# Performance work log

Hardware: AMD Instinct MI355X
Metric: run time of the kernel (lower is better)

## Reference

```python
import jax, jax.numpy as jnp
import numpy as np

B, C_IN, H, W = 4, 1536, 64, 64   # SGI input: cat of three 512-ch encoder maps at 64x64
HID, OUT = 1536, 512
N = H * W


def _grid_edge_index(h, w):
    # 4-connected bidirectional grid, matching SGI.grid_edge_index
    idx = np.arange(h * w).reshape(h, w)
    right = np.stack([idx[:, :-1].ravel(), idx[:, 1:].ravel()])
    down = np.stack([idx[:-1, :].ravel(), idx[1:, :].ravel()])
    ei = np.concatenate([right, down, right[::-1], down[::-1]], axis=1)
    return ei.astype(np.int32)


def setup_inputs() -> dict:
    key = jax.random.key(0)
    ks = jax.random.split(key, 7)
    ei = _grid_edge_index(H, W)
    s = 0.02
    return {
        "x":  jax.random.normal(ks[0], (B, C_IN, H, W), jnp.float32),
        "W1": jax.random.normal(ks[1], (C_IN, HID), jnp.float32) * s,
        "b1": jnp.zeros((HID,), jnp.float32),
        "W2": jax.random.normal(ks[2], (HID, OUT), jnp.float32) * s,
        "b2": jnp.zeros((OUT,), jnp.float32),
        "Wl": jax.random.normal(ks[3], (C_IN, OUT), jnp.float32) * s,
        "bl": jnp.zeros((OUT,), jnp.float32),
        "src": jnp.asarray(ei[0]),
        "dst": jnp.asarray(ei[1]),
    }


def _gcn(h_in, Wt, b, src, dst, inv_sqrt_deg, inv_deg):
    # PyG GCNConv: lin -> symmetric-normalized aggregation (with self loops) -> +bias
    h = h_in @ Wt                                   # [B, N, F]
    norm = inv_sqrt_deg[src] * inv_sqrt_deg[dst]    # [E]
    msgs = h[:, src, :] * norm[None, :, None]       # [B, E, F]
    # self-loop contribution has norm 1/deg_i
    agg = (h * inv_deg[None, :, None]).at[:, dst, :].add(msgs)
    return agg + b


def reference(x, W1, b1, W2, b2, Wl, bl, src, dst):
    Bb, C, Hh, Ww = x.shape
    n = Hh * Ww
    # degree including self loop (graph is symmetric)
    deg = jnp.zeros((n,), x.dtype).at[dst].add(1.0) + 1.0
    inv_sqrt_deg = jax.lax.rsqrt(deg)
    inv_deg = 1.0 / deg

    xt = x.reshape(Bb, C, n).transpose(0, 2, 1)     # [B, N, C]
    identity = xt
    origin = xt @ Wl + bl                           # [B, N, OUT]
    h = jax.nn.relu(_gcn(xt, W1, b1, src, dst, inv_sqrt_deg, inv_deg))
    h = _gcn(h + identity, W2, b2, src, dst, inv_sqrt_deg, inv_deg)
    out = h * origin                                # [B, N, OUT]
    return out.transpose(0, 2, 1).reshape(Bb, out.shape[-1], Hh, Ww)
```

## Files before the change

kernel.cpp:

```cpp
#include <hip/hip_runtime.h>
#include <hip/hip_bf16.h>
#include <stdint.h>


typedef __bf16 bf16;
typedef float f32x4 __attribute__((ext_vector_type(4)));
typedef bf16 bf16x8 __attribute__((ext_vector_type(8)));

#define NB 4
#define NN 4096
#define CIN 1536
#define HIDF 1536
#define OUTF 512

__device__ __forceinline__ float rs_of(int gx, int gy) {
  const int d = (gx > 0) + (gx < 63) + (gy > 0) + (gy < 63);
  return d == 2 ? 0.57735027f : (d == 3 ? 0.5f : 0.44721360f);
}

#define XBLK 1536
#define W1BLK 576
#define W2BLK 192

__global__ __launch_bounds__(256) void prep(
    const float* __restrict__ x, const float* __restrict__ W1,
    const float* __restrict__ W2, const float* __restrict__ Wl,
    bf16* __restrict__ xt, bf16* __restrict__ xa, bf16* __restrict__ w1t,
    bf16* __restrict__ w2t, bf16* __restrict__ wlt) {
  __shared__ float vt[64 * 64];
  __shared__ float at[64 * 64];
  const int B = blockIdx.x, t = threadIdx.x;
  const int tx = t & 15, ty = t >> 4;
  const int lane = t & 63, w = t >> 6;
  const int u = lane & 7, n3 = lane >> 3;

  if (B < XBLK) {
    const int yb = (B & 7) * 2 + ((B >> 3) & 1);
    const int rest = B >> 4;
    const int ct = rest % 24, bb = rest / 24;
    const int c0 = ct * 64;
    const float* xb = x + (long)bb * CIN * NN;
    const float* rowb = xb + (long)(c0 + ty * 4) * NN + tx * 4;
    bf16* xtb = xt + (long)bb * NN * CIN;
    bf16* xab = xa + (long)bb * NN * CIN;

    f32x4 vup[4], vcur[4], vdn[4];
    const int gy0 = yb * 4;
    if (gy0 > 0) {
#pragma unroll
      for (int cc = 0; cc < 4; cc++)
        vup[cc] = *(const f32x4*)(rowb + (long)cc * NN + (long)(gy0 - 1) * 64);
    } else {
#pragma unroll
      for (int cc = 0; cc < 4; cc++) vup[cc] = {0.f, 0.f, 0.f, 0.f};
    }
#pragma unroll
    for (int cc = 0; cc < 4; cc++)
      vcur[cc] = *(const f32x4*)(rowb + (long)cc * NN + (long)gy0 * 64);
#pragma unroll
    for (int cc = 0; cc < 4; cc++)
      vdn[cc] = *(const f32x4*)(rowb + (long)cc * NN + (long)(gy0 + 1) * 64);

#pragma unroll
    for (int s = 0; s < 4; s++) {
      const int gy = yb * 4 + s;
      const int n0 = gy * 64;
      float lf[4], rt[4];
#pragma unroll
      for (int cc = 0; cc < 4; cc++) {
        lf[cc] = __shfl_up(vcur[cc][3], 1);
        rt[cc] = __shfl_down(vcur[cc][0], 1);
      }
#pragma unroll
      for (int cc = 0; cc < 4; cc++) {
        const int cl = ty * 4 + cc;
        const int nb = tx * 4;
        f32x4 a;
#pragma unroll
        for (int i = 0; i < 4; i++) {
          const int gx = nb + i;
          const float rs_s = rs_of(gx, gy);
          const float lv = (i == 0) ? lf[cc] : vcur[cc][i - 1];
          const float rv = (i == 3) ? rt[cc] : vcur[cc][i + 1];
          float sum = vcur[cc][i] * rs_s;
          if (gx > 0) sum += lv * rs_of(gx - 1, gy);
          if (gx < 63) sum += rv * rs_of(gx + 1, gy);
          if (gy > 0) sum += vup[cc][i] * rs_of(gx, gy - 1);
          if (gy < 63) sum += vdn[cc][i] * rs_of(gx, gy + 1);
          a[i] = rs_s * sum;
        }
        const int chunk = tx ^ (2 * ((cl >> 3) & 7));
        *(f32x4*)&vt[cl * 64 + chunk * 4] = vcur[cc];
        *(f32x4*)&at[cl * 64 + chunk * 4] = a;
      }
      f32x4 vnext[4];
      if (s < 3) {
        const int gn = gy + 2;
        if (gn <= 63) {
#pragma unroll
          for (int cc = 0; cc < 4; cc++)
            vnext[cc] =
                *(const f32x4*)(rowb + (long)cc * NN + (long)gn * 64);
        } else {
#pragma unroll
          for (int cc = 0; cc < 4; cc++) vnext[cc] = {0.f, 0.f, 0.f, 0.f};
        }
      }
      __syncthreads();
#pragma unroll
      for (int q = 0; q < 4; q++) {
        const int j = q * 4 + w;
        const int arr = j & 1, r2 = j >> 1;
        const int nl = n3 + 8 * r2;
        const float* sp = arr ? at : vt;
        bf16x8 o;
#pragma unroll
        for (int jj = 0; jj < 8; jj++) {
          const int cl = u * 8 + jj;
          const int col = nl ^ (8 * ((cl >> 3) & 7));
          o[jj] = (bf16)sp[cl * 64 + col];
        }
        bf16* outp = arr ? xab : xtb;
        *(bf16x8*)&outp[(long)(n0 + nl) * CIN + c0 + u * 8] = o;
      }
      if (s < 3) {
        __syncthreads();
#pragma unroll
        for (int cc = 0; cc < 4; cc++) {
          vup[cc] = vcur[cc];
          vcur[cc] = vdn[cc];
          vdn[cc] = vnext[cc];
        }
      }
    }
  } else {
    int B2 = B - XBLK;
    const float* srcp;
    bf16* dstp;
    int Fdim, Kd, nt, ct;
    if (B2 < W1BLK) {
      nt = B2 / 24; ct = B2 % 24; srcp = W1; dstp = w1t; Fdim = HIDF; Kd = CIN;
    } else if (B2 < W1BLK + W2BLK) {
      const int l = B2 - W1BLK;
      nt = l / 24; ct = l % 24; srcp = W2; dstp = w2t; Fdim = OUTF; Kd = HIDF;
    } else {
      const int l = B2 - W1BLK - W2BLK;
      nt = l / 24; ct = l % 24; srcp = Wl; dstp = wlt; Fdim = OUTF; Kd = CIN;
    }
    const int n0 = nt * 64, c0 = ct * 64;
#pragma unroll
    for (int cc = 0; cc < 4; cc++) {
      const int cl = ty * 4 + cc;
      const float* row = srcp + (long)(c0 + cl) * Fdim + n0;
      f32x4 v = *(const f32x4*)(row + tx * 4);
      const int chunk = tx ^ (2 * ((cl >> 3) & 7));
      *(f32x4*)&vt[cl * 64 + chunk * 4] = v;
    }
    __syncthreads();
#pragma unroll
    for (int q = 0; q < 2; q++) {
      const int r = q * 4 + w;
      const int nl = n3 + 8 * r;
      bf16x8 o;
#pragma unroll
      for (int jj = 0; jj < 8; jj++) {
        const int cl = u * 8 + jj;
        const int col = nl ^ (8 * ((cl >> 3) & 7));
        o[jj] = (bf16)vt[cl * 64 + col];
      }
      *(bf16x8*)&dstp[(long)(n0 + nl) * Kd + c0 + u * 8] = o;
    }
  }
}

__device__ __forceinline__ void async_copy16(const void* g, void* l) {
  __builtin_amdgcn_global_load_lds(
      (const __attribute__((address_space(1))) void*)g,
      (__attribute__((address_space(3))) void*)l, 16, 0, 0);
}

struct GemmCtx {
  f32x4 acc[4][4];
  int wave, lane, wm, wn, quad, l15;
};

__device__ __forceinline__ void gemm_init(GemmCtx& cx, int t) {
  cx.wave = t >> 6;
  cx.lane = t & 63;
  cx.wm = (cx.wave & 1) * 64;
  cx.wn = (cx.wave >> 1) * 64;
  cx.quad = cx.lane >> 4;
  cx.l15 = cx.lane & 15;
#pragma unroll
  for (int i = 0; i < 4; i++)
#pragma unroll
    for (int j = 0; j < 4; j++) cx.acc[i][j] = {0.f, 0.f, 0.f, 0.f};
}

template <int K>
__device__ __forceinline__ void gemm_kloop(GemmCtx& cx, const bf16* Ab,
                                           const bf16* Bb, bf16* As,
                                           bf16* Bs) {
  const int r = cx.lane >> 3, c8 = cx.lane & 7;
  const int fchunk = c8 ^ r;
  constexpr int NT = K / 64;
#pragma unroll
  for (int i = 0; i < 4; i++) {
    const int row = i * 32 + cx.wave * 8;
    async_copy16(Ab + (long)(row + r) * K + fchunk * 8, &As[row * 64]);
    async_copy16(Bb + (long)(row + r) * K + fchunk * 8, &Bs[row * 64]);
  }
  __syncthreads();
#pragma unroll 2
  for (int t = 0; t < NT; ++t) {
    const int cur = (t & 1) * (128 * 64);
    const int nxt = cur ^ (128 * 64);
    const int ktn = ((t + 1 < NT) ? t + 1 : t) * 64;
#pragma unroll
    for (int i = 0; i < 4; i++) {
      const int row = i * 32 + cx.wave * 8;
      async_copy16(Ab + (long)(row + r) * K + ktn + fchunk * 8,
                   &As[nxt + row * 64]);
      async_copy16(Bb + (long)(row + r) * K + ktn + fchunk * 8,
                   &Bs[nxt + row * 64]);
    }
#pragma unroll
    for (int kk = 0; kk < 2; kk++) {
      const int q = kk * 4 + cx.quad;
      bf16x8 af[4], bfv[4];
#pragma unroll
      for (int mr = 0; mr < 4; mr++) {
        const int m = cx.wm + mr * 16 + cx.l15;
        af[mr] = *(const bf16x8*)&As[cur + m * 64 + (q ^ (m & 7)) * 8];
      }
#pragma unroll
      for (int nc = 0; nc < 4; nc++) {
        const int n = cx.wn + nc * 16 + cx.l15;
        bfv[nc] = *(const bf16x8*)&Bs[cur + n * 64 + (q ^ (n & 7)) * 8];
      }
#pragma unroll
      for (int mr = 0; mr < 4; mr++)
#pragma unroll
        for (int nc = 0; nc < 4; nc++)
          cx.acc[mr][nc] = __builtin_amdgcn_mfma_f32_16x16x32_bf16(
              af[mr], bfv[nc], cx.acc[mr][nc], 0, 0, 0);
    }
    __syncthreads();
  }
}

__global__ __launch_bounds__(256) void gemm_h(
    const bf16* __restrict__ xa, const bf16* __restrict__ w1t,
    const bf16* __restrict__ xt, bf16* __restrict__ h,
    const float* __restrict__ b1) {
  __shared__ bf16 As[2 * 128 * 64];
  __shared__ bf16 Bs[2 * 128 * 64];
  GemmCtx cx;
  gemm_init(cx, threadIdx.x);
  const int m0 = blockIdx.x * 128, n0 = blockIdx.y * 128, z = blockIdx.z;
  gemm_kloop<CIN>(cx, xa + (long)z * NN * CIN + (long)m0 * CIN,
                  w1t + (long)n0 * CIN, As, Bs);
  const bf16* Xb = xt + (long)z * NN * HIDF;
  bf16* Cb = h + (long)z * NN * HIDF;
#pragma unroll
  for (int mr = 0; mr < 4; mr++)
#pragma unroll
    for (int nc = 0; nc < 4; nc++) {
      const int gn = n0 + cx.wn + nc * 16 + cx.l15;
      const float bv = b1[gn];
#pragma unroll
      for (int j = 0; j < 4; j++) {
        const int gm = m0 + cx.wm + mr * 16 + cx.quad * 4 + j;
        float v = cx.acc[mr][nc][j] + bv;
        v = v > 0.f ? v : 0.f;
        Cb[(long)gm * HIDF + gn] = (bf16)(v + (float)Xb[(long)gm * HIDF + gn]);
      }
    }
}

template <bool ADD_BIAS>
__global__ __launch_bounds__(256) void gemm_f32(
    const bf16* __restrict__ A, const bf16* __restrict__ Bw,
    float* __restrict__ C, const float* __restrict__ bias) {
  __shared__ bf16 As[2 * 128 * 64];
  __shared__ bf16 Bs[2 * 128 * 64];
  GemmCtx cx;
  gemm_init(cx, threadIdx.x);
  const int m0 = blockIdx.x * 128, n0 = blockIdx.y * 128, z = blockIdx.z;
  gemm_kloop<CIN>(cx, A + (long)z * NN * CIN + (long)m0 * CIN,
                  Bw + (long)n0 * CIN, As, Bs);
  float* Cb = C + (long)z * NN * OUTF;
#pragma unroll
  for (int mr = 0; mr < 4; mr++)
#pragma unroll
    for (int nc = 0; nc < 4; nc++) {
      const int gn = n0 + cx.wn + nc * 16 + cx.l15;
      float bv = 0.f;
      if (ADD_BIAS) bv = bias[gn];
#pragma unroll
      for (int j = 0; j < 4; j++) {
        const int gm = m0 + cx.wm + mr * 16 + cx.quad * 4 + j;
        Cb[(long)gm * OUTF + gn] = cx.acc[mr][nc][j] + bv;
      }
    }
}

__global__ __launch_bounds__(256) void stencil2(
    const float* __restrict__ G2, const float* __restrict__ Orig,
    const float* __restrict__ b2, float* __restrict__ out) {
  __shared__ float tile[16][516];
  const int blk = blockIdx.x;
  const int s = ((blk & 7) << 5) + (blk >> 3);
  const int n0 = s * 16, b = blockIdx.y;
  const int t = threadIdx.x;
  const int fq = t & 127, nl = t >> 7;
  const int f = fq * 4;
  const f32x4 bv = *(const f32x4*)(b2 + f);
#pragma unroll
  for (int p = 0; p < 8; p++) {
    const int nLoc = p * 2 + nl;
    const int n = n0 + nLoc;
    const int gx = n & 63, gy = n >> 6;
    const float rs_n = rs_of(gx, gy);
    const long rb = ((long)b * NN + n) * (long)OUTF + f;
    f32x4 g = *(const f32x4*)(G2 + rb);
    f32x4 a;
#pragma unroll
    for (int i = 0; i < 4; i++) a[i] = g[i] * rs_n;
    if (gx > 0) {
      const float w = rs_of(gx - 1, gy);
      f32x4 u = *(const f32x4*)(G2 + rb - OUTF);
#pragma unroll
      for (int i = 0; i < 4; i++) a[i] += u[i] * w;
    }
    if (gx < 63) {
      const float w = rs_of(gx + 1, gy);
      f32x4 u = *(const f32x4*)(G2 + rb + OUTF);
#pragma unroll
      for (int i = 0; i < 4; i++) a[i] += u[i] * w;
    }
    if (gy > 0) {
      const float w = rs_of(gx, gy - 1);
      f32x4 u = *(const f32x4*)(G2 + rb - 64L * OUTF);
#pragma unroll
      for (int i = 0; i < 4; i++) a[i] += u[i] * w;
    }
    if (gy < 63) {
      const float w = rs_of(gx, gy + 1);
      f32x4 u = *(const f32x4*)(G2 + rb + 64L * OUTF);
#pragma unroll
      for (int i = 0; i < 4; i++) a[i] += u[i] * w;
    }
    f32x4 og = *(const f32x4*)(Orig + rb);
    f32x4 res;
#pragma unroll
    for (int i = 0; i < 4; i++) res[i] = (a[i] * rs_n + bv[i]) * og[i];
    *(f32x4*)&tile[nLoc][f] = res;
  }
  __syncthreads();
  const int j = t & 3, fr = t >> 2;
#pragma unroll
  for (int q = 0; q < 8; q++) {
    const int ff = q * 64 + fr;
    f32x4 v;
#pragma unroll
    for (int k = 0; k < 4; k++) v[k] = tile[j * 4 + k][ff];
    *(f32x4*)&out[((long)b * OUTF + ff) * (long)NN + n0 + j * 4] = v;
  }
}

extern "C" void kernel_launch(void* const* d_in, const int* in_sizes, int n_in,
                              void* d_out, int out_size, void* d_ws,
                              size_t ws_size, hipStream_t stream) {
  const float* x = (const float*)d_in[0];
  const float* W1 = (const float*)d_in[1];
  const float* b1 = (const float*)d_in[2];
  const float* W2 = (const float*)d_in[3];
  const float* b2 = (const float*)d_in[4];
  const float* Wl = (const float*)d_in[5];
  const float* bl = (const float*)d_in[6];
  float* out = (float*)d_out;

  uint8_t* ws = (uint8_t*)d_ws;
  size_t off = 0;
  auto alloc = [&](size_t bytes) -> void* {
    void* p = ws + off;
    off += (bytes + 255) & ~(size_t)255;
    return p;
  };
  bf16* xt = (bf16*)alloc((size_t)NB * NN * CIN * 2);
  bf16* xa = (bf16*)alloc((size_t)NB * NN * CIN * 2);
  bf16* hb = (bf16*)alloc((size_t)NB * NN * HIDF * 2);
  bf16* w1t = (bf16*)alloc((size_t)HIDF * CIN * 2);
  bf16* w2t = (bf16*)alloc((size_t)OUTF * HIDF * 2);
  bf16* wlt = (bf16*)alloc((size_t)OUTF * CIN * 2);
  float* origin = (float*)xa;
  float* g2 = (float*)xt;

  prep<<<XBLK + W1BLK + 2 * W2BLK, 256, 0, stream>>>(x, W1, W2, Wl, xt, xa,
                                                     w1t, w2t, wlt);
  gemm_h<<<dim3(NN / 128, HIDF / 128, NB), 256, 0, stream>>>(xa, w1t, xt, hb,
                                                             b1);
  gemm_f32<true><<<dim3(NN / 128, OUTF / 128, NB), 256, 0, stream>>>(
      xt, wlt, origin, bl);
  gemm_f32<false><<<dim3(NN / 128, OUTF / 128, NB), 256, 0, stream>>>(
      hb, w2t, g2, nullptr);
  stencil2<<<dim3(256, NB), 256, 0, stream>>>(g2, origin, b2, out);
}
```

Baseline: 370.2 us.

## Prefetch two K-tiles ahead with explicit vmcnt waits in GEMM k-loop

Restructures the double-buffered GEMM main loop so that two K-tiles are issued before the loop and each iteration refills the buffer it just consumed with tile t+2. Instead of a full __syncthreads, it waits with s_waitcnt vmcnt(8) so only the older tile's async copies must land. The aim is to keep a whole tile of global loads in flight during the MFMA work and hide memory latency. It relies on hand-placed barriers and counter waits, so the correctness of the buffer reuse depends on the exact count of async copies per tile.

```diff
diff --git a/kernel.cpp b/kernel.cpp
--- a/kernel.cpp
+++ b/kernel.cpp
@@ -197,6 +197,8 @@
     for (int j = 0; j < 4; j++) cx.acc[i][j] = {0.f, 0.f, 0.f, 0.f};
 }
 
+#define TS (128 * 64)
+
 template <int K>
 __device__ __forceinline__ void gemm_kloop(GemmCtx& cx, const bf16* Ab,
                                            const bf16* Bb, bf16* As,
@@ -204,57 +206,72 @@
   const int r = cx.lane >> 3, c8 = cx.lane & 7;
   const int fchunk = c8 ^ r;
   constexpr int NT = K / 64;
+  static_assert(K >= 128, "pipeline needs >=2 K-tiles");
 #pragma unroll
   for (int i = 0; i < 4; i++) {
     const int row = i * 32 + cx.wave * 8;
     async_copy16(Ab + (long)(row + r) * K + fchunk * 8, &As[row * 64]);
     async_copy16(Bb + (long)(row + r) * K + fchunk * 8, &Bs[row * 64]);
   }
-  __syncthreads();
+#pragma unroll
+  for (int i = 0; i < 4; i++) {
+    const int row = i * 32 + cx.wave * 8;
+    async_copy16(Ab + (long)(row + r) * K + 64 + fchunk * 8,
+                 &As[TS + row * 64]);
+    async_copy16(Bb + (long)(row + r) * K + 64 + fchunk * 8,
+                 &Bs[TS + row * 64]);
+  }
 #pragma unroll 2
   for (int t = 0; t < NT; ++t) {
-    const int cur = (t & 1) * (128 * 64);
-    const int nxt = cur ^ (128 * 64);
-    const int ktn = ((t + 1 < NT) ? t + 1 : t) * 64;
+    const int cur = (t & 1) * TS;
+    asm volatile("s_waitcnt vmcnt(8)" ::: "memory");
+    __builtin_amdgcn_s_barrier();
+    __builtin_amdgcn_sched_barrier(0);
+#pragma unroll
+    for (int kk = 0; kk < 2; kk++) {
+      const int q = kk * 4 + cx.quad;
+      bf16x8 af[4], bfv[4];
+#pragma unroll
+      for (int mr = 0; mr < 4; mr++) {
+        const int m = cx.wm + mr * 16 + cx.l15;
+        af[mr] = *(const bf16x8*)&As[cur + m * 64 + (q ^ (m & 7)) * 8];
+      }
+#pragma unroll
+      for (int nc = 0; nc < 4; nc++) {
+        const int n = cx.wn + nc * 16 + cx.l15;
+        bfv[nc] = *(const bf16x8*)&Bs[cur + n * 64 + (q ^ (n & 7)) * 8];
+      }
+#pragma unroll
+      for (int mr = 0; mr < 4; mr++)
+#pragma unroll
+        for (int nc = 0; nc < 4; nc++)
+          cx.acc[mr][nc] = __builtin_amdgcn_mfma_f32_16x16x32_bf16(
+              af[mr], bfv[nc], cx.acc[mr][nc], 0, 0, 0);
+    }
+    asm volatile("s_waitcnt lgkmcnt(0)" ::: "memory");
+    __builtin_amdgcn_sched_barrier(0);
+    __builtin_amdgcn_s_barrier();
+    __builtin_amdgcn_sched_barrier(0);
+    const int ktn = (t + 2 < NT ? t + 2 : NT - 1) * 64;
 #pragma unroll
     for (int i = 0; i < 4; i++) {
       const int row = i * 32 + cx.wave * 8;
       async_copy16(Ab + (long)(row + r) * K + ktn + fchunk * 8,
-                   &As[nxt + row * 64]);
+                   &As[cur + row * 64]);
       async_copy16(Bb + (long)(row + r) * K + ktn + fchunk * 8,
-                   &Bs[nxt + row * 64]);
-    }
-#pragma unroll
-    for (int kk = 0; kk < 2; kk++) {
-      const int q = kk * 4 + cx.quad;
-      bf16x8 af[4], bfv[4];
-#pragma unroll
-      for (int mr = 0; mr < 4; mr++) {
-        const int m = cx.wm + mr * 16 + cx.l15;
-        af[mr] = *(const bf16x8*)&As[cur + m * 64 + (q ^ (m & 7)) * 8];
-      }
-#pragma unroll
-      for (int nc = 0; nc < 4; nc++) {
-        const int n = cx.wn + nc * 16 + cx.l15;
-        bfv[nc] = *(const bf16x8*)&Bs[cur + n * 64 + (q ^ (n & 7)) * 8];
-      }
-#pragma unroll
-      for (int mr = 0; mr < 4; mr++)
-#pragma unroll
-        for (int nc = 0; nc < 4; nc++)
-          cx.acc[mr][nc] = __builtin_amdgcn_mfma_f32_16x16x32_bf16(
-              af[mr], bfv[nc], cx.acc[mr][nc], 0, 0, 0);
-    }
-    __syncthreads();
-  }
+                   &Bs[cur + row * 64]);
+    }
+    __builtin_amdgcn_sched_barrier(0);
+  }
+  asm volatile("s_waitcnt vmcnt(0)" ::: "memory");
 }
 
 __global__ __launch_bounds__(256) void gemm_h(
     const bf16* __restrict__ xa, const bf16* __restrict__ w1t,
     const bf16* __restrict__ xt, bf16* __restrict__ h,
     const float* __restrict__ b1) {
-  __shared__ bf16 As[2 * 128 * 64];
-  __shared__ bf16 Bs[2 * 128 * 64];
+  __shared__ bf16 As[2 * TS];
+  __shared__ bf16 Bs[2 * TS];
   GemmCtx cx;
   gemm_init(cx, threadIdx.x);
   const int m0 = blockIdx.x * 128, n0 = blockIdx.y * 128, z = blockIdx.z;
@@ -282,8 +299,8 @@
 __global__ __launch_bounds__(256) void gemm_f32(
     const bf16* __restrict__ A, const bf16* __restrict__ Bw,
     float* __restrict__ C, const float* __restrict__ bias) {
-  __shared__ bf16 As[2 * 128 * 64];
-  __shared__ bf16 Bs[2 * 128 * 64];
+  __shared__ bf16 As[2 * TS];
+  __shared__ bf16 Bs[2 * TS];
   GemmCtx cx;
   gemm_init(cx, threadIdx.x);
   const int m0 = blockIdx.x * 128, n0 = blockIdx.y * 128, z = blockIdx.z;
```

Result: faster. 360.6 us (-2.6%).
